# Optimization experiments

Measured on AMD Instinct MI355X. Metric: run time of the kernel, lower is better.

The kernel has to match this reference:

```python
import jax, jax.numpy as jnp
import numpy as np

N_NODES = 20000
N_EDGES = 320000
HIDDEN = 64
HEADS = 4
D_INNER = 256
NEG_SLOPE = 0.2
BN_EPS = 1e-5


def setup_inputs() -> dict:
    key = jax.random.key(0)
    ks = jax.random.split(key, 8)
    s = 1.0 / np.sqrt(HIDDEN)
    return {
        "x": jax.random.normal(ks[0], (N_NODES, HIDDEN), jnp.float32),
        "edge_index": jax.random.randint(ks[1], (2, N_EDGES), 0, N_NODES, jnp.int64),
        "W_l": jax.random.normal(ks[2], (HIDDEN, HEADS * HIDDEN), jnp.float32) * s,
        "b_l": jnp.zeros((HEADS * HIDDEN,), jnp.float32),
        "W_r": jax.random.normal(ks[3], (HIDDEN, HEADS * HIDDEN), jnp.float32) * s,
        "b_r": jnp.zeros((HEADS * HIDDEN,), jnp.float32),
        "att": jax.random.normal(ks[4], (HEADS, HIDDEN), jnp.float32) * s,
        "bias_gat": jnp.zeros((HIDDEN,), jnp.float32),
        "gamma1": jnp.ones((HIDDEN,), jnp.float32),
        "beta1": jnp.zeros((HIDDEN,), jnp.float32),
        "W1": jax.random.normal(ks[5], (HIDDEN, D_INNER), jnp.float32) * s,
        "b1": jnp.zeros((D_INNER,), jnp.float32),
        "W2": jax.random.normal(ks[6], (D_INNER, HIDDEN), jnp.float32) / np.sqrt(D_INNER),
        "b2": jnp.zeros((HIDDEN,), jnp.float32),
        "gamma2": jnp.ones((HIDDEN,), jnp.float32),
        "beta2": jnp.zeros((HIDDEN,), jnp.float32),
    }


def _batch_norm(x, gamma, beta):
    # training-mode BatchNorm1d over the node axis (biased variance, as torch)
    mu = x.mean(0)
    var = jnp.mean((x - mu) ** 2, axis=0)
    return (x - mu) * jax.lax.rsqrt(var + BN_EPS) * gamma + beta


def _gatv2(x, edge_index, W_l, b_l, W_r, b_r, att, bias_gat):
    N = x.shape[0]
    H, C = att.shape
    src, dst = edge_index[0], edge_index[1]  # j (source), i (target)
    xl = (x @ W_l + b_l).reshape(N, H, C)  # messages (x_j side)
    xr = (x @ W_r + b_r).reshape(N, H, C)  # target (x_i side)
    # GATv2 dynamic attention: a^T LeakyReLU(x_i + x_j), per head
    e = jax.nn.leaky_relu(xl[src] + xr[dst], NEG_SLOPE)  # [E, H, C]
    score = jnp.einsum("ehc,hc->eh", e, att)  # [E, H]
    # segment softmax over incoming edges of each target node
    m = jax.ops.segment_max(score, dst, num_segments=N)  # [N, H]
    ex = jnp.exp(score - m[dst])
    denom = jax.ops.segment_sum(ex, dst, num_segments=N)  # [N, H]
    alpha = ex / jnp.maximum(denom[dst], 1e-16)  # [E, H]
    out = jax.ops.segment_sum(alpha[:, :, None] * xl[src], dst, num_segments=N)  # [N, H, C]
    return out.mean(axis=1) + bias_gat  # concat=False -> mean over heads


def reference(x, edge_index, W_l, b_l, W_r, b_r, att, bias_gat,
              gamma1, beta1, W1, b1, W2, b2, gamma2, beta2):
    x2 = _gatv2(x, edge_index, W_l, b_l, W_r, b_r, att, bias_gat)
    x = x + x2  # dropout is identity in eval
    x = _batch_norm(x, gamma1, beta1)
    ff = jax.nn.relu(x @ W1 + b1) @ W2 + b2
    x = x + ff
    x = _batch_norm(x, gamma2, beta2)
    return x
```

## Files before the change

kernel.cpp:

```cpp
#include <hip/hip_runtime.h>
#include <hip/hip_bf16.h>
#include <math.h>

#define N_NODES 20000
#define N_EDGES 320000
#define HIDDEN 64
#define HEADS 4
#define HC 256
#define D_INNER 256
#define NEG_SLOPE 0.2f
#define BN_EPS 1e-5f
#define MAXDEG 64
#define NZERO (N_NODES + 2048)
#define NB_LIN 626
#define NB_FILL 1250

typedef __attribute__((ext_vector_type(8))) short short8;
typedef __attribute__((ext_vector_type(4))) float f32x4;

__device__ __forceinline__ float bf2f(unsigned short u) {
    unsigned x = ((unsigned)u) << 16;
    return __uint_as_float(x);
}
__device__ __forceinline__ unsigned short f2bf(float f) {
    __hip_bfloat16 b = __float2bfloat16(f);
    return *reinterpret_cast<unsigned short*>(&b);
}
__device__ __forceinline__ void cvt8(uint4 u, float* f) {
    f[0] = __uint_as_float(u.x << 16); f[1] = __uint_as_float(u.x & 0xFFFF0000u);
    f[2] = __uint_as_float(u.y << 16); f[3] = __uint_as_float(u.y & 0xFFFF0000u);
    f[4] = __uint_as_float(u.z << 16); f[5] = __uint_as_float(u.z & 0xFFFF0000u);
    f[6] = __uint_as_float(u.w << 16); f[7] = __uint_as_float(u.w & 0xFFFF0000u);
}

__global__ __launch_bounds__(256) void k_wprep(const float* __restrict__ W1, const float* __restrict__ W2,
                                               const float* __restrict__ Wl, const float* __restrict__ Wr,
                                               unsigned short* __restrict__ W1tb, unsigned short* __restrict__ W2tb,
                                               unsigned short* __restrict__ Wlrtb,
                                               int* __restrict__ zbuf, int* __restrict__ perm) {
    int idx = blockIdx.x * 256 + threadIdx.x;
    if (idx < NZERO) zbuf[idx] = 0;
    int4 z4 = {0, 0, 0, 0};
    int4* p4 = (int4*)perm;
#pragma unroll
    for (int i = 0; i < 5; ++i) {
        int k = idx + i * 65536;
        if (k < N_NODES * MAXDEG / 4) p4[k] = z4;
    }
    if (idx < 16384) {
        int k = idx >> 8, n = idx & 255;
        W1tb[n * 64 + k] = f2bf(W1[idx]);
    } else if (idx < 32768) {
        int j = idx - 16384;
        int k = j >> 6, n = j & 63;
        W2tb[n * 256 + k] = f2bf(W2[j]);
    } else if (idx < 49152) {
        int j = idx - 32768;
        int k = j >> 8, n = j & 255;
        Wlrtb[n * 64 + k] = f2bf(Wl[j]);
    } else {
        int j = idx - 49152;
        int k = j >> 8, n = j & 255;
        Wlrtb[16384 + n * 64 + k] = f2bf(Wr[j]);
    }
}

__global__ __launch_bounds__(256) void k_prep(const float* __restrict__ x,
                                              const unsigned short* __restrict__ Wlrtb,
                                              const float* __restrict__ bl, const float* __restrict__ br,
                                              unsigned short* __restrict__ xlb, unsigned short* __restrict__ xrb,
                                              const int* __restrict__ ei,
                                              int* __restrict__ cursor, int* __restrict__ perm) {
    __shared__ unsigned short sW[16384];
    int t = threadIdx.x;
    if (blockIdx.x >= NB_LIN) {
        int e = (blockIdx.x - NB_LIN) * 256 + t;
        int ed = ei[N_EDGES + e];
        int slot = atomicAdd(&cursor[ed], 1);
        perm[ed * MAXDEG + slot] = ei[e];
        return;
    }
    int w = t >> 6, lane = t & 63;
    int l15 = lane & 15, lg = lane >> 4;
    int side = blockIdx.x & 1;
    int row0 = (blockIdx.x >> 1) * 64;
    const float* bias = side ? br : bl;
    unsigned short* dst = side ? xrb : xlb;
    {
        const short8* src = (const short8*)(Wlrtb + side * 16384);
#pragma unroll
        for (int it = 0; it < 8; ++it) {
            int i = it * 256 + t;
            int n = i >> 3, c = i & 7;
            *(short8*)((char*)sW + n * 128 + ((c * 16) ^ ((n & 7) << 4))) = src[i];
        }
    }
    short8 af[4][2];
#pragma unroll
    for (int mt = 0; mt < 4; ++mt) {
        int gm = row0 + mt * 16 + l15;
        bool valid = gm < N_NODES;
#pragma unroll
        for (int kk = 0; kk < 2; ++kk) {
            int k0 = kk * 32 + lg * 8;
            float4 v0 = {0.f,0.f,0.f,0.f}, v1 = {0.f,0.f,0.f,0.f};
            if (valid) {
                v0 = *(const float4*)(x + (size_t)gm * 64 + k0);
                v1 = *(const float4*)(x + (size_t)gm * 64 + k0 + 4);
            }
            short8 f;
            f[0] = (short)f2bf(v0.x); f[1] = (short)f2bf(v0.y);
            f[2] = (short)f2bf(v0.z); f[3] = (short)f2bf(v0.w);
            f[4] = (short)f2bf(v1.x); f[5] = (short)f2bf(v1.y);
            f[6] = (short)f2bf(v1.z); f[7] = (short)f2bf(v1.w);
            af[mt][kk] = f;
        }
    }
    float bv[4];
#pragma unroll
    for (int nt = 0; nt < 4; ++nt) bv[nt] = bias[w * 64 + nt * 16 + l15];
    __syncthreads();
    f32x4 zero4 = {0.f, 0.f, 0.f, 0.f};
    f32x4 acc[4][4];
#pragma unroll
    for (int mt = 0; mt < 4; ++mt)
#pragma unroll
        for (int nt = 0; nt < 4; ++nt) acc[mt][nt] = zero4;
#pragma unroll
    for (int kk = 0; kk < 2; ++kk) {
        int kb = kk * 64 + lg * 16;
        short8 bf[4];
#pragma unroll
        for (int nt = 0; nt < 4; ++nt) {
            int n = w * 64 + nt * 16 + l15;
            bf[nt] = *(const short8*)((const char*)sW + n * 128 + (kb ^ ((n & 7) << 4)));
        }
#pragma unroll
        for (int mt = 0; mt < 4; ++mt)
#pragma unroll
            for (int nt = 0; nt < 4; ++nt)
                acc[mt][nt] = __builtin_amdgcn_mfma_f32_16x16x32_bf16(af[mt][kk], bf[nt], acc[mt][nt], 0, 0, 0);
    }
#pragma unroll
    for (int mt = 0; mt < 4; ++mt)
#pragma unroll
        for (int nt = 0; nt < 4; ++nt) {
            int n = w * 64 + nt * 16 + l15;
#pragma unroll
            for (int r = 0; r < 4; ++r) {
                int gm = row0 + mt * 16 + lg * 4 + r;
                if (gm < N_NODES)
                    dst[(size_t)gm * 256 + n] = f2bf(acc[mt][nt][r] + bv[nt]);
            }
        }
}

__global__ __launch_bounds__(256) void k_gat(const unsigned short* __restrict__ xlb,
                                             const unsigned short* __restrict__ xrb,
                                             const float* __restrict__ att,
                                             const int* __restrict__ perm,
                                             const int* __restrict__ cnt,
                                             const float* __restrict__ x,
                                             const float* __restrict__ bias,
                                             float* __restrict__ y1,
                                             float* __restrict__ gsum, float* __restrict__ gsq) {
    __shared__ float ps[8][64], pq[8][64];
    int t = threadIdx.x;
    int hw = t >> 5, l = t & 31;
    int node = blockIdx.x * 8 + hw;
    const uint4* xl4 = (const uint4*)xlb;
    uint4 xru = ((const uint4*)xrb)[(size_t)node * 32 + l];
    float xr[8]; cvt8(xru, xr);
    float at[8];
    *(float4*)(at)     = *(const float4*)(att + l * 8);
    *(float4*)(at + 4) = *(const float4*)(att + l * 8 + 4);
    int deg = cnt[node];
    int mdeg = max(deg, __shfl_xor(deg, 32));
    const int* ep = perm + (size_t)node * MAXDEG;
    float d = 0.f;
    float acc[8] = {0.f,0.f,0.f,0.f,0.f,0.f,0.f,0.f};
    uint4 b0 = xl4[(size_t)ep[0] * 32 + l];
    uint4 b1 = xl4[(size_t)ep[1] * 32 + l];
    uint4 b2 = xl4[(size_t)ep[2] * 32 + l];
    uint4 b3 = xl4[(size_t)ep[3] * 32 + l];
    for (int j = 0; j < mdeg; j += 2) {
        uint4 n0 = xl4[(size_t)ep[j + 4] * 32 + l];
        uint4 n1 = xl4[(size_t)ep[j + 5] * 32 + l];
        float xl0[8], xl1[8];
        cvt8(b0, xl0); cvt8(b1, xl1);
        float sv0 = 0.f, sa0 = 0.f, sv1 = 0.f, sa1 = 0.f;
#pragma unroll
        for (int i = 0; i < 8; ++i) {
            float v0 = xl0[i] + xr[i];
            float v1 = xl1[i] + xr[i];
            sv0 = fmaf(at[i], v0, sv0);
            sa0 = fmaf(at[i], fabsf(v0), sa0);
            sv1 = fmaf(at[i], v1, sv1);
            sa1 = fmaf(at[i], fabsf(v1), sa1);
        }
        float s0 = 0.6f * sv0 + 0.4f * sa0;
        float s1 = 0.6f * sv1 + 0.4f * sa1;
        s0 += __shfl_xor(s0, 1); s1 += __shfl_xor(s1, 1);
        s0 += __shfl_xor(s0, 2); s1 += __shfl_xor(s1, 2);
        s0 += __shfl_xor(s0, 4); s1 += __shfl_xor(s1, 4);
        float w0 = (j < deg)     ? __expf(s0) : 0.f;
        float w1 = (j + 1 < deg) ? __expf(s1) : 0.f;
        d += w0 + w1;
#pragma unroll
        for (int i = 0; i < 8; ++i)
            acc[i] = fmaf(w0, xl0[i], fmaf(w1, xl1[i], acc[i]));
        b0 = b2; b1 = b3; b2 = n0; b3 = n1;
    }
    float inv = 1.f / fmaxf(d, 1e-16f);
#pragma unroll
    for (int i = 0; i < 8; ++i) {
        float v2 = acc[i] * inv;
        v2 += __shfl_xor(v2, 8);
        v2 += __shfl_xor(v2, 16);
        acc[i] = v2;
    }
    if (l < 8) {
        float4 xv0 = *(const float4*)(x + (size_t)node * 64 + l * 8);
        float4 xv1 = *(const float4*)(x + (size_t)node * 64 + l * 8 + 4);
        float4 bv0 = *(const float4*)(bias + l * 8);
        float4 bv1 = *(const float4*)(bias + l * 8 + 4);
        float4 y0, y1v;
        y0.x = xv0.x + 0.25f * acc[0] + bv0.x;
        y0.y = xv0.y + 0.25f * acc[1] + bv0.y;
        y0.z = xv0.z + 0.25f * acc[2] + bv0.z;
        y0.w = xv0.w + 0.25f * acc[3] + bv0.w;
        y1v.x = xv1.x + 0.25f * acc[4] + bv1.x;
        y1v.y = xv1.y + 0.25f * acc[5] + bv1.y;
        y1v.z = xv1.z + 0.25f * acc[6] + bv1.z;
        y1v.w = xv1.w + 0.25f * acc[7] + bv1.w;
        *(float4*)(y1 + (size_t)node * 64 + l * 8) = y0;
        *(float4*)(y1 + (size_t)node * 64 + l * 8 + 4) = y1v;
        int c = l * 8;
        ps[hw][c+0] = y0.x; ps[hw][c+1] = y0.y; ps[hw][c+2] = y0.z; ps[hw][c+3] = y0.w;
        ps[hw][c+4] = y1v.x; ps[hw][c+5] = y1v.y; ps[hw][c+6] = y1v.z; ps[hw][c+7] = y1v.w;
        pq[hw][c+0] = y0.x*y0.x; pq[hw][c+1] = y0.y*y0.y; pq[hw][c+2] = y0.z*y0.z; pq[hw][c+3] = y0.w*y0.w;
        pq[hw][c+4] = y1v.x*y1v.x; pq[hw][c+5] = y1v.y*y1v.y; pq[hw][c+6] = y1v.z*y1v.z; pq[hw][c+7] = y1v.w*y1v.w;
    }
    __syncthreads();
    if (t < 64) {
        float s = 0.f, q = 0.f;
#pragma unroll
        for (int r = 0; r < 8; ++r) { s += ps[r][t]; q += pq[r][t]; }
        int rb = blockIdx.x & 7;
        atomicAdd(&gsum[rb * 64 + t], s);
        atomicAdd(&gsq [rb * 64 + t], q);
    }
}

__global__ __launch_bounds__(256) void k_ffn(const float* __restrict__ y1,
                                             const float* __restrict__ s1, const float* __restrict__ q1,
                                             const float* __restrict__ gamma1, const float* __restrict__ beta1,
                                             const unsigned short* __restrict__ W1tb, const float* __restrict__ b1,
                                             const unsigned short* __restrict__ W2tb, const float* __restrict__ b2,
                                             float* __restrict__ out,
                                             float* __restrict__ gsum2, float* __restrict__ gsq2) {
    __shared__ unsigned short sW[16384];
    __shared__ unsigned short sH[16384];
    __shared__ __align__(16) float sA1[64], sC1[64];
    int t = threadIdx.x;
    int w = t >> 6, lane = t & 63;
    int l15 = lane & 15, lg = lane >> 4;
    int blk = blockIdx.x;

    {
        const short8* src = (const short8*)W1tb;
#pragma unroll
        for (int it = 0; it < 8; ++it) {
            int i = it * 256 + t;
            int n = i >> 3, c = i & 7;
            *(short8*)((char*)sW + n * 128 + ((c * 16) ^ ((n & 7) << 4))) = src[i];
        }
    }
    if (t < 64) {
        float s = 0.f, q = 0.f;
#pragma unroll
        for (int r = 0; r < 8; ++r) { s += s1[r * 64 + t]; q += q1[r * 64 + t]; }
        float mu = s * (1.0f / N_NODES);
        float var = fmaxf(q * (1.0f / N_NODES) - mu * mu, 0.f);
        float av = gamma1[t] * rsqrtf(var + BN_EPS);
        sA1[t] = av; sC1[t] = beta1[t] - mu * av;
    }
    __syncthreads();

    float4 a1k[2][2], c1k[2][2];
#pragma unroll
    for (int kk = 0; kk < 2; ++kk) {
        int k0 = kk * 32 + lg * 8;
        a1k[kk][0] = *(const float4*)(sA1 + k0); a1k[kk][1] = *(const float4*)(sA1 + k0 + 4);
        c1k[kk][0] = *(const float4*)(sC1 + k0); c1k[kk][1] = *(const float4*)(sC1 + k0 + 4);
    }
    short8 af[4][2];
#pragma unroll
    for (int mt = 0; mt < 4; ++mt) {
        int gm = blk * 64 + mt * 16 + l15;
        bool valid = gm < N_NODES;
#pragma unroll
        for (int kk = 0; kk < 2; ++kk) {
            int k0 = kk * 32 + lg * 8;
            float4 v0 = {0.f,0.f,0.f,0.f}, v1 = {0.f,0.f,0.f,0.f};
            if (valid) {
                v0 = *(const float4*)(y1 + (size_t)gm * 64 + k0);
                v1 = *(const float4*)(y1 + (size_t)gm * 64 + k0 + 4);
            }
            short8 f;
            f[0] = (short)f2bf(fmaf(a1k[kk][0].x, v0.x, c1k[kk][0].x));
            f[1] = (short)f2bf(fmaf(a1k[kk][0].y, v0.y, c1k[kk][0].y));
            f[2] = (short)f2bf(fmaf(a1k[kk][0].z, v0.z, c1k[kk][0].z));
            f[3] = (short)f2bf(fmaf(a1k[kk][0].w, v0.w, c1k[kk][0].w));
            f[4] = (short)f2bf(fmaf(a1k[kk][1].x, v1.x, c1k[kk][1].x));
            f[5] = (short)f2bf(fmaf(a1k[kk][1].y, v1.y, c1k[kk][1].y));
            f[6] = (short)f2bf(fmaf(a1k[kk][1].z, v1.z, c1k[kk][1].z));
            f[7] = (short)f2bf(fmaf(a1k[kk][1].w, v1.w, c1k[kk][1].w));
            af[mt][kk] = f;
        }
    }
    float b1v[4];
#pragma unroll
    for (int nt = 0; nt < 4; ++nt) b1v[nt] = b1[w * 64 + nt * 16 + l15];

    f32x4 zero4 = {0.f, 0.f, 0.f, 0.f};
    f32x4 acc[4][4];
#pragma unroll
    for (int mt = 0; mt < 4; ++mt)
#pragma unroll
        for (int nt = 0; nt < 4; ++nt) acc[mt][nt] = zero4;
#pragma unroll
    for (int kk = 0; kk < 2; ++kk) {
        int kb = kk * 64 + lg * 16;
        short8 bf[4];
#pragma unroll
        for (int nt = 0; nt < 4; ++nt) {
            int n = w * 64 + nt * 16 + l15;
            bf[nt] = *(const short8*)((const char*)sW + n * 128 + (kb ^ ((n & 7) << 4)));
        }
#pragma unroll
        for (int mt = 0; mt < 4; ++mt)
#pragma unroll
            for (int nt = 0; nt < 4; ++nt)
                acc[mt][nt] = __builtin_amdgcn_mfma_f32_16x16x32_bf16(af[mt][kk], bf[nt], acc[mt][nt], 0, 0, 0);
    }
    __syncthreads();

#pragma unroll
    for (int mt = 0; mt < 4; ++mt)
#pragma unroll
        for (int nt = 0; nt < 4; ++nt) {
            int n = w * 64 + nt * 16 + l15;
#pragma unroll
            for (int r = 0; r < 4; ++r) {
                int m = mt * 16 + lg * 4 + r;
                float h = fmaxf(acc[mt][nt][r] + b1v[nt], 0.f);
                *(unsigned short*)((char*)sH + m * 512 + ((n * 2) ^ ((m & 7) << 4))) = f2bf(h);
            }
        }
    {
        const short8* src = (const short8*)W2tb;
#pragma unroll
        for (int it = 0; it < 8; ++it) {
            int i = it * 256 + t;
            int n = i >> 5, c = i & 31;
            *(short8*)((char*)sW + n * 512 + ((c * 16) ^ ((n & 7) << 4))) = src[i];
        }
    }
    __syncthreads();

    f32x4 acc2[4];
#pragma unroll
    for (int nt = 0; nt < 4; ++nt) acc2[nt] = zero4;
#pragma unroll
    for (int kk = 0; kk < 8; ++kk) {
        int kb = kk * 64 + lg * 16;
        int m = w * 16 + l15;
        short8 a2 = *(const short8*)((const char*)sH + m * 512 + (kb ^ ((m & 7) << 4)));
#pragma unroll
        for (int nt = 0; nt < 4; ++nt) {
            int n = nt * 16 + l15;
            short8 b2f = *(const short8*)((const char*)sW + n * 512 + (kb ^ ((n & 7) << 4)));
            acc2[nt] = __builtin_amdgcn_mfma_f32_16x16x32_bf16(a2, b2f, acc2[nt], 0, 0, 0);
        }
    }

    float b2v[4], a1n[4], c1n[4], ssum[4] = {0.f,0.f,0.f,0.f}, ssq[4] = {0.f,0.f,0.f,0.f};
#pragma unroll
    for (int nt = 0; nt < 4; ++nt) {
        int n = nt * 16 + l15;
        b2v[nt] = b2[n]; a1n[nt] = sA1[n]; c1n[nt] = sC1[n];
    }
#pragma unroll
    for (int nt = 0; nt < 4; ++nt) {
        int n = nt * 16 + l15;
#pragma unroll
        for (int r = 0; r < 4; ++r) {
            int gm = blk * 64 + w * 16 + lg * 4 + r;
            if (gm < N_NODES) {
                float v = acc2[nt][r] + b2v[nt] + fmaf(a1n[nt], y1[(size_t)gm * 64 + n], c1n[nt]);
                out[(size_t)gm * 64 + n] = v;
                ssum[nt] += v; ssq[nt] += v * v;
            }
        }
    }
    __syncthreads();
    float* fs = (float*)sW;
#pragma unroll
    for (int nt = 0; nt < 4; ++nt) {
        float ss = ssum[nt], qq = ssq[nt];
        ss += __shfl_xor(ss, 16); ss += __shfl_xor(ss, 32);
        qq += __shfl_xor(qq, 16); qq += __shfl_xor(qq, 32);
        if (lg == 0) {
            int n = nt * 16 + l15;
            fs[w * 64 + n] = ss;
            fs[256 + w * 64 + n] = qq;
        }
    }
    __syncthreads();
    if (t < 64) {
        int r = blk & 7;
        atomicAdd(&gsum2[r * 64 + t], fs[t] + fs[64 + t] + fs[128 + t] + fs[192 + t]);
        atomicAdd(&gsq2 [r * 64 + t], fs[256 + t] + fs[320 + t] + fs[384 + t] + fs[448 + t]);
    }
}

__global__ __launch_bounds__(256) void k_apply(float* __restrict__ out,
                                               const float* __restrict__ s2, const float* __restrict__ q2,
                                               const float* __restrict__ gamma2, const float* __restrict__ beta2) {
    __shared__ float sA[64], sC[64];
    int t = threadIdx.x;
    if (t < 64) {
        float s = 0.f, q = 0.f;
#pragma unroll
        for (int r = 0; r < 8; ++r) { s += s2[r * 64 + t]; q += q2[r * 64 + t]; }
        float mu = s * (1.0f / N_NODES);
        float var = fmaxf(q * (1.0f / N_NODES) - mu * mu, 0.f);
        float av = gamma2[t] * rsqrtf(var + BN_EPS);
        sA[t] = av; sC[t] = beta2[t] - mu * av;
    }
    __syncthreads();
    int idx = blockIdx.x * 1024 + t * 4;
    int ch = (t & 15) * 4;
    float4 v = *(float4*)(out + idx);
    v.x = fmaf(sA[ch+0], v.x, sC[ch+0]);
    v.y = fmaf(sA[ch+1], v.y, sC[ch+1]);
    v.z = fmaf(sA[ch+2], v.z, sC[ch+2]);
    v.w = fmaf(sA[ch+3], v.w, sC[ch+3]);
    *(float4*)(out + idx) = v;
}

extern "C" void kernel_launch(void* const* d_in, const int* in_sizes, int n_in,
                              void* d_out, int out_size, void* d_ws, size_t ws_size,
                              hipStream_t stream) {
    const float* x        = (const float*)d_in[0];
    const int*   ei       = (const int*)d_in[1];
    const float* Wl       = (const float*)d_in[2];
    const float* bl       = (const float*)d_in[3];
    const float* Wr       = (const float*)d_in[4];
    const float* br       = (const float*)d_in[5];
    const float* att      = (const float*)d_in[6];
    const float* bias_gat = (const float*)d_in[7];
    const float* gamma1   = (const float*)d_in[8];
    const float* beta1    = (const float*)d_in[9];
    const float* W1       = (const float*)d_in[10];
    const float* b1       = (const float*)d_in[11];
    const float* W2       = (const float*)d_in[12];
    const float* b2       = (const float*)d_in[13];
    const float* gamma2   = (const float*)d_in[14];
    const float* beta2    = (const float*)d_in[15];
    float* out = (float*)d_out;

    char* ws = (char*)d_ws;
    unsigned short* xlb = (unsigned short*)ws;
    unsigned short* xrb = xlb + (size_t)N_NODES * HC;
    float* y1    = (float*)(xrb + (size_t)N_NODES * HC);
    int*   perm  = (int*)(y1 + (size_t)N_NODES * HIDDEN);
    int*   cursor= perm + (size_t)N_NODES * MAXDEG;
    float* stats = (float*)(cursor + N_NODES);
    unsigned short* W1tb  = (unsigned short*)(stats + 2048);
    unsigned short* W2tb  = W1tb + 16384;
    unsigned short* Wlrtb = W2tb + 16384;

    k_wprep<<<256, 256, 0, stream>>>(W1, W2, Wl, Wr, W1tb, W2tb, Wlrtb, cursor, perm);
    k_prep <<<NB_LIN + NB_FILL, 256, 0, stream>>>(x, Wlrtb, bl, br, xlb, xrb, ei, cursor, perm);
    k_gat  <<<N_NODES / 8, 256, 0, stream>>>(xlb, xrb, att, perm, cursor, x, bias_gat, y1,
                                             stats + 0, stats + 512);
    k_ffn  <<<(N_NODES + 63) / 64, 256, 0, stream>>>(y1, stats + 0, stats + 512, gamma1, beta1,
                                                     W1tb, b1, W2tb, b2, out,
                                                     stats + 1024, stats + 1536);
    k_apply<<<N_NODES * HIDDEN / 1024, 256, 0, stream>>>(out, stats + 1024, stats + 1536, gamma2, beta2);
}
```

Before: 85.37 us.

## Skip perm zero-fill with index clamping; read W2 directly from global in FFN

Removes the zero-initialisation of the 5 MB perm adjacency buffer in the weight-prep kernel. The GAT kernel instead clamps out-of-range neighbour indices when prefetching, so uninitialised padding slots read a valid row whose weight is masked anyway. The FFN kernel no longer stages W2 into shared memory: the second GEMM loads B fragments straight from global/L2, which removes a copy and two barriers. The risk is that garbage indices might be valid-looking values, and that repeated global loads of W2 cost more than the removed staging. Dropping the barrier before reusing sW for the stats reduction may be a race unless the earlier sync covers it.

```diff
diff --git a/kernel.cpp b/kernel.cpp
--- a/kernel.cpp
+++ b/kernel.cpp
@@ -32,21 +32,17 @@
     f[4] = __uint_as_float(u.z << 16); f[5] = __uint_as_float(u.z & 0xFFFF0000u);
     f[6] = __uint_as_float(u.w << 16); f[7] = __uint_as_float(u.w & 0xFFFF0000u);
 }
+__device__ __forceinline__ int clampi(int v) {
+    return ((unsigned)v < (unsigned)N_NODES) ? v : 0;
+}
 
 __global__ __launch_bounds__(256) void k_wprep(const float* __restrict__ W1, const float* __restrict__ W2,
                                                const float* __restrict__ Wl, const float* __restrict__ Wr,
                                                unsigned short* __restrict__ W1tb, unsigned short* __restrict__ W2tb,
                                                unsigned short* __restrict__ Wlrtb,
-                                               int* __restrict__ zbuf, int* __restrict__ perm) {
+                                               int* __restrict__ zbuf) {
     int idx = blockIdx.x * 256 + threadIdx.x;
     if (idx < NZERO) zbuf[idx] = 0;
-    int4 z4 = {0, 0, 0, 0};
-    int4* p4 = (int4*)perm;
-#pragma unroll
-    for (int i = 0; i < 5; ++i) {
-        int k = idx + i * 65536;
-        if (k < N_NODES * MAXDEG / 4) p4[k] = z4;
-    }
     if (idx < 16384) {
         int k = idx >> 8, n = idx & 255;
         W1tb[n * 64 + k] = f2bf(W1[idx]);
@@ -179,13 +175,13 @@
     const int* ep = perm + (size_t)node * MAXDEG;
     float d = 0.f;
     float acc[8] = {0.f,0.f,0.f,0.f,0.f,0.f,0.f,0.f};
-    uint4 b0 = xl4[(size_t)ep[0] * 32 + l];
-    uint4 b1 = xl4[(size_t)ep[1] * 32 + l];
-    uint4 b2 = xl4[(size_t)ep[2] * 32 + l];
-    uint4 b3 = xl4[(size_t)ep[3] * 32 + l];
+    uint4 b0 = xl4[(size_t)clampi(ep[0]) * 32 + l];
+    uint4 b1 = xl4[(size_t)clampi(ep[1]) * 32 + l];
+    uint4 b2 = xl4[(size_t)clampi(ep[2]) * 32 + l];
+    uint4 b3 = xl4[(size_t)clampi(ep[3]) * 32 + l];
     for (int j = 0; j < mdeg; j += 2) {
-        uint4 n0 = xl4[(size_t)ep[j + 4] * 32 + l];
-        uint4 n1 = xl4[(size_t)ep[j + 5] * 32 + l];
+        uint4 n0 = xl4[(size_t)clampi(ep[j + 4]) * 32 + l];
+        uint4 n1 = xl4[(size_t)clampi(ep[j + 5]) * 32 + l];
         float xl0[8], xl1[8];
         cvt8(b0, xl0); cvt8(b1, xl1);
         float sv0 = 0.f, sa0 = 0.f, sv1 = 0.f, sa1 = 0.f;
@@ -344,7 +340,6 @@
             for (int nt = 0; nt < 4; ++nt)
                 acc[mt][nt] = __builtin_amdgcn_mfma_f32_16x16x32_bf16(af[mt][kk], bf[nt], acc[mt][nt], 0, 0, 0);
     }
-    __syncthreads();
 
 #pragma unroll
     for (int mt = 0; mt < 4; ++mt)
@@ -358,15 +353,6 @@
                 *(unsigned short*)((char*)sH + m * 512 + ((n * 2) ^ ((m & 7) << 4))) = f2bf(h);
             }
         }
-    {
-        const short8* src = (const short8*)W2tb;
-#pragma unroll
-        for (int it = 0; it < 8; ++it) {
-            int i = it * 256 + t;
-            int n = i >> 5, c = i & 31;
-            *(short8*)((char*)sW + n * 512 + ((c * 16) ^ ((n & 7) << 4))) = src[i];
-        }
-    }
     __syncthreads();
 
     f32x4 acc2[4];
@@ -380,7 +366,7 @@
 #pragma unroll
         for (int nt = 0; nt < 4; ++nt) {
             int n = nt * 16 + l15;
-            short8 b2f = *(const short8*)((const char*)sW + n * 512 + (kb ^ ((n & 7) << 4)));
+            short8 b2f = *(const short8*)(W2tb + n * 256 + (kb >> 1));
             acc2[nt] = __builtin_amdgcn_mfma_f32_16x16x32_bf16(a2, b2f, acc2[nt], 0, 0, 0);
         }
     }
@@ -404,7 +390,6 @@
             }
         }
     }
-    __syncthreads();
     float* fs = (float*)sW;
 #pragma unroll
     for (int nt = 0; nt < 4; ++nt) {
@@ -482,7 +467,7 @@
     unsigned short* W2tb  = W1tb + 16384;
     unsigned short* Wlrtb = W2tb + 16384;
 
-    k_wprep<<<256, 256, 0, stream>>>(W1, W2, Wl, Wr, W1tb, W2tb, Wlrtb, cursor, perm);
+    k_wprep<<<256, 256, 0, stream>>>(W1, W2, Wl, Wr, W1tb, W2tb, Wlrtb, cursor);
     k_prep <<<NB_LIN + NB_FILL, 256, 0, stream>>>(x, Wlrtb, bl, br, xlb, xrb, ei, cursor, perm);
     k_gat  <<<N_NODES / 8, 256, 0, stream>>>(xlb, xrb, att, perm, cursor, x, bias_gat, y1,
                                              stats + 0, stats + 512);
```

Result: slower. 96.15 us (+12.6%).
